# Optimization experiments

Measured on AMD Instinct MI355X. Metric: run time of the kernel, lower is better.

The kernel has to match this reference:

```python
import jax, jax.numpy as jnp
import numpy as np


def setup_inputs() -> dict:
    key = jax.random.key(0)
    ks = jax.random.split(key, 10)
    B, S, I, Hy, H = 16, 4096, 256, 64, 512
    sc = 0.05
    return {
        "x": jax.random.normal(ks[0], (B, S, I), jnp.float32),
        "hidden": jax.random.normal(ks[1], (B, H), jnp.float32),
        "lin0_W": jax.random.normal(ks[2], (Hy, I), jnp.float32) * sc,
        "lin0_b": jax.random.normal(ks[3], (Hy,), jnp.float32) * sc,
        "sig0_W": jax.random.normal(ks[4], (Hy, I), jnp.float32) * sc,
        "sig0_b": jax.random.normal(ks[5], (Hy,), jnp.float32) * sc,
        "fch_W": jax.random.normal(ks[6], (H, Hy), jnp.float32) * sc,
        "fch_b": jax.random.normal(ks[7], (H,), jnp.float32) * sc,
        "fc2_W": jax.random.normal(ks[8], (H, I), jnp.float32) * sc,
        "fc2_b": jax.random.normal(ks[9], (H,), jnp.float32) * sc,
    }


def reference(x, hidden, lin0_W, lin0_b, sig0_W, sig0_b, fch_W, fch_b, fc2_W, fc2_b):
    # GLN sub-network (num_layers=1): relu(linear(x) * sigmoid(linear(x)))
    lin = jnp.einsum('bsi,hi->bsh', x, lin0_W) + lin0_b          # [B,S,Hy]
    gate = jax.nn.sigmoid(jnp.einsum('bsi,hi->bsh', x, sig0_W) + sig0_b)
    g = jax.nn.relu(lin * gate)                                   # [B,S,Hy]
    b = jnp.einsum('bsh,dh->bsd', g, fch_W) + fch_b               # [B,S,H]
    # multihead gating
    sig_alphas = jax.nn.sigmoid(jnp.einsum('bsi,di->bsd', x, fc2_W) + fc2_b)
    b = b * sig_alphas

    # sequential recurrence: h_t = relu(b_t + roll(h_{t-1}, 1, -1)); h_{-1} = hidden
    def step(h, b_t):
        h = jax.nn.relu(b_t + jnp.roll(h, 1, axis=-1))
        return h, h

    b_tmajor = jnp.swapaxes(b, 0, 1)  # [S,B,H]
    last, outs = jax.lax.scan(step, hidden, b_tmajor)
    outputs = jnp.swapaxes(outs, 0, 1)  # [B,S,H]
    return outputs, last
```

## Files before the change

### kernel.cpp

```cpp
#include <hip/hip_runtime.h>

typedef __attribute__((ext_vector_type(4))) float  f32x4;
typedef __attribute__((ext_vector_type(4))) short  s16x4;
typedef __attribute__((ext_vector_type(8))) short  s16x8;
typedef __bf16 bf16x8 __attribute__((ext_vector_type(8)));

#define NBATCH 16
#define SEQ    4096
#define KIN    256
#define HY     64
#define HOUT   512
#define NROWS  (NBATCH*SEQ)
#define LC     32
#define NC     (SEQ/LC)

#define GP(x) ((const __attribute__((address_space(1))) void*)(x))
#define LP(x) ((__attribute__((address_space(3))) void*)(x))

static __device__ __forceinline__ short f2bf(float f) {
  unsigned u = __float_as_uint(f);
  u = u + 0x7FFF + ((u >> 16) & 1);
  return (short)(u >> 16);
}
static __device__ __forceinline__ float bf2f(short h) {
  return __uint_as_float(((unsigned)(unsigned short)h) << 16);
}
static __device__ __forceinline__ f32x4 mfma16(bf16x8 a, bf16x8 b, f32x4 c) {
  return __builtin_amdgcn_mfma_f32_16x16x32_bf16(a, b, c, 0, 0, 0);
}
static __device__ __forceinline__ bf16x8 ldfrag(const short* p) {
  return *reinterpret_cast<const bf16x8*>(p);
}
static __device__ __forceinline__ float fsigmoid(float z) {
  return 1.f / (1.f + __expf(-z));
}

__global__ void prep_w(const float* __restrict__ lin0W, const float* __restrict__ sig0W,
                       const float* __restrict__ fchW,  const float* __restrict__ fc2W,
                       short* __restrict__ W1h, short* __restrict__ W2h,
                       short* __restrict__ Fh,  short* __restrict__ F2h) {
  int i = blockIdx.x * 256 + threadIdx.x;
  if (i < 16384) {
    W1h[i] = f2bf(lin0W[i]);
    W2h[i] = f2bf(sig0W[i]);
  } else if (i < 16384 + 32768) {
    Fh[i - 16384] = f2bf(fchW[i - 16384]);
  } else if (i < 16384 + 32768 + 131072) {
    F2h[i - 49152] = f2bf(fc2W[i - 49152]);
  }
}

__global__ __launch_bounds__(256) void gx(
    const float* __restrict__ x,
    const short* __restrict__ W1h, const short* __restrict__ W2h,
    const float* __restrict__ lin0b, const float* __restrict__ sig0b,
    short* __restrict__ Gh, short* __restrict__ xh) {
  __shared__ __align__(16) short smem[64 * 256 + 64 * 64];
  short* Ah = smem;
  short* gL = smem + 64 * 256;
  int tid = threadIdx.x;
  int row0 = blockIdx.x * 64;
  #pragma unroll
  for (int i = 0; i < 8; ++i) {
    int slot = i * 256 + tid;
    int r = slot >> 5, k8 = slot & 31;
    const float* xp = x + (size_t)(row0 + r) * KIN + k8 * 8;
    f32x4 v0 = *reinterpret_cast<const f32x4*>(xp);
    f32x4 v1 = *reinterpret_cast<const f32x4*>(xp + 4);
    s16x8 hh;
    #pragma unroll
    for (int j = 0; j < 4; ++j) { hh[j] = f2bf(v0[j]); hh[4 + j] = f2bf(v1[j]); }
    *reinterpret_cast<s16x8*>(&Ah[(r * 256 + k8 * 8) ^ ((r & 7) << 3)]) = hh;
    *reinterpret_cast<s16x8*>(xh + (size_t)(row0 + r) * KIN + k8 * 8) = hh;
  }
  __syncthreads();
  int w = tid >> 6, l = tid & 63, lr = l & 15, lg = l >> 4;
  {
    int c = w * 16 + lr;
    f32x4 a1[4], a2[4];
    #pragma unroll
    for (int rt = 0; rt < 4; ++rt) { a1[rt] = (f32x4)0.f; a2[rt] = (f32x4)0.f; }
    #pragma unroll
    for (int ks = 0; ks < 8; ++ks) {
      int kk = ks * 32 + lg * 8;
      bf16x8 b1 = ldfrag(W1h + c * 256 + kk);
      bf16x8 b2 = ldfrag(W2h + c * 256 + kk);
      #pragma unroll
      for (int rt = 0; rt < 4; ++rt) {
        int r = rt * 16 + lr;
        bf16x8 a = ldfrag(&Ah[(r * 256 + kk) ^ ((r & 7) << 3)]);
        a1[rt] = mfma16(b1, a, a1[rt]);
        a2[rt] = mfma16(b2, a, a2[rt]);
      }
    }
    f32x4 blv = *reinterpret_cast<const f32x4*>(lin0b + w * 16 + lg * 4);
    f32x4 bsv = *reinterpret_cast<const f32x4*>(sig0b + w * 16 + lg * 4);
    #pragma unroll
    for (int rt = 0; rt < 4; ++rt) {
      int xrl = rt * 16 + lr;
      s16x4 gg;
      #pragma unroll
      for (int j = 0; j < 4; ++j) {
        float g = (a1[rt][j] + blv[j]) * fsigmoid(a2[rt][j] + bsv[j]);
        gg[j] = f2bf(g > 0.f ? g : 0.f);
      }
      *reinterpret_cast<s16x4*>(&gL[(xrl * 64 + w * 16 + lg * 4) ^ ((xrl & 7) << 3)]) = gg;
    }
  }
  __syncthreads();
  #pragma unroll
  for (int i = 0; i < 2; ++i) {
    int slot = i * 256 + tid;
    int row = slot >> 3, c8 = slot & 7;
    s16x8 v = *reinterpret_cast<const s16x8*>(&gL[(row * 64 + c8 * 8) ^ ((row & 7) << 3)]);
    *reinterpret_cast<s16x8*>(Gh + (size_t)(row0 + row) * HY + c8 * 8) = v;
  }
}

__global__ __launch_bounds__(512, 4) void bg(
    const short* __restrict__ xh, const short* __restrict__ Gh,
    const short* __restrict__ F2h, const short* __restrict__ Fh,
    const float* __restrict__ fchb, const float* __restrict__ fc2b,
    short* __restrict__ Bb) {
  __shared__ __align__(16) short smem[2][16384];
  short* bT = &smem[0][0];
  int tid = threadIdx.x;
  int w = tid >> 6, l = tid & 63;
  int lr = l & 15, lg = l >> 4;
  int r0 = (w >> 1) * 32;
  int c0 = (w & 1) * 64;
  int bid = blockIdx.x;
  int xcd = bid & 7, idx = bid >> 3;
  int colTile = xcd >> 1;
  int rowTile = ((xcd & 1) << 8) + idx;
  int row0 = rowTile * 128;
  int col0 = colTile * 128;

  auto stage = [&](int t, int b) {
    short* As = &smem[b][0];
    short* Bs = &smem[b][8192];
    #pragma unroll
    for (int j = 0; j < 2; ++j) {
      int blk = w * 2 + j;
      int flat = blk * 64 + l;
      int row = flat >> 3, sp = flat & 7;
      int seg = sp ^ (row & 7);
      const short* asrc = (t < 4) ? xh + (size_t)(row0 + row) * KIN + t * 64 + seg * 8
                                  : Gh + (size_t)(row0 + row) * HY + seg * 8;
      const short* bsrc = (t < 4) ? F2h + (size_t)(col0 + row) * KIN + t * 64 + seg * 8
                                  : Fh + (size_t)(col0 + row) * HY + seg * 8;
      __builtin_amdgcn_global_load_lds(GP(asrc), LP(&As[blk * 512]), 16, 0, 0);
      __builtin_amdgcn_global_load_lds(GP(bsrc), LP(&Bs[blk * 512]), 16, 0, 0);
    }
  };
  auto compute = [&](int b, f32x4 (&acc)[2][4]) {
    short* As = &smem[b][0];
    short* Bs = &smem[b][8192];
    #pragma unroll
    for (int ksl = 0; ksl < 2; ++ksl) {
      bf16x8 Af[2], Bf[4];
      #pragma unroll
      for (int i = 0; i < 2; ++i) {
        int row = r0 + i * 16 + lr;
        Af[i] = ldfrag(&As[row * 64 + ((ksl * 32 + lg * 8) ^ ((row & 7) << 3))]);
      }
      #pragma unroll
      for (int i = 0; i < 4; ++i) {
        int col = c0 + i * 16 + lr;
        Bf[i] = ldfrag(&Bs[col * 64 + ((ksl * 32 + lg * 8) ^ ((col & 7) << 3))]);
      }
      #pragma unroll
      for (int rt = 0; rt < 2; ++rt)
        #pragma unroll
        for (int ct = 0; ct < 4; ++ct)
          acc[rt][ct] = mfma16(Af[rt], Bf[ct], acc[rt][ct]);
    }
  };

  f32x4 acc2[2][4], accF[2][4];
  #pragma unroll
  for (int rt = 0; rt < 2; ++rt)
    #pragma unroll
    for (int ct = 0; ct < 4; ++ct) { acc2[rt][ct] = (f32x4)0.f; accF[rt][ct] = (f32x4)0.f; }

  stage(0, 0);
  __syncthreads();
  #pragma unroll
  for (int t = 0; t < 5; ++t) {
    if (t < 4) stage(t + 1, (t + 1) & 1);
    if (t < 4) compute(t & 1, acc2);
    else       compute(t & 1, accF);
    __syncthreads();
  }

  #pragma unroll
  for (int ct = 0; ct < 4; ++ct) {
    int lc = c0 + ct * 16 + lr;
    int col = col0 + lc;
    float bc = fchb[col], b2c = fc2b[col];
    #pragma unroll
    for (int rt = 0; rt < 2; ++rt) {
      int tl0 = r0 + rt * 16 + lg * 4;
      #pragma unroll
      for (int j = 0; j < 4; ++j) {
        int tl = tl0 + j;
        float alpha = fsigmoid(acc2[rt][ct][j] + b2c);
        bT[(tl * 128 + lc) ^ ((tl & 7) << 3)] = f2bf((accF[rt][ct][j] + bc) * alpha);
      }
    }
  }
  __syncthreads();
  #pragma unroll
  for (int i = 0; i < 4; ++i) {
    int slot = i * 512 + tid;
    int row = slot >> 4, c8 = slot & 15;
    s16x8 vv = *reinterpret_cast<const s16x8*>(&bT[(row * 128 + c8 * 8) ^ ((row & 7) << 3)]);
    *reinterpret_cast<s16x8*>(Bb + (size_t)(row0 + row) * HOUT + col0 + c8 * 8) = vv;
  }
}

__global__ __launch_bounds__(64) void scan_passA(const short* __restrict__ Bb,
                                                 float* __restrict__ Cc, float* __restrict__ Sc) {
  int bc = blockIdx.x;
  int l = threadIdx.x;
  int row0 = bc * LC;
  const short* bp = Bb + (size_t)row0 * HOUT + l * 8;
  s16x8 v0 = *reinterpret_cast<const s16x8*>(bp);
  float C[8], S[8];
  #pragma unroll
  for (int i = 0; i < 8; ++i) { S[i] = bf2f(v0[i]); C[i] = 0.f; }
  s16x8 vc = *reinterpret_cast<const s16x8*>(bp + (size_t)HOUT);
  for (int t = 1; t < LC; ++t) {
    s16x8 vn;
    if (t + 1 < LC) vn = *reinterpret_cast<const s16x8*>(bp + (size_t)(t + 1) * HOUT);
    float bb[8];
    #pragma unroll
    for (int i = 0; i < 8; ++i) bb[i] = bf2f(vc[i]);
    float pC = __shfl(C[7], (l + 63) & 63);
    float pS = __shfl(S[7], (l + 63) & 63);
    #pragma unroll
    for (int i = 7; i >= 1; --i) { C[i] = fmaxf(0.f, bb[i] + C[i - 1]); S[i] = bb[i] + S[i - 1]; }
    C[0] = fmaxf(0.f, bb[0] + pC);
    S[0] = bb[0] + pS;
    vc = vn;
  }
  float* cp = Cc + (size_t)bc * HOUT + l * 8;
  float* sp = Sc + (size_t)bc * HOUT + l * 8;
  #pragma unroll
  for (int i = 0; i < 8; ++i) { cp[i] = C[i]; sp[i] = S[i]; }
}

__global__ __launch_bounds__(64) void scan_combine(const float* __restrict__ hidden,
                                                   const float* __restrict__ Cc, const float* __restrict__ Sc,
                                                   float* __restrict__ hIn, float* __restrict__ lastOut) {
  int batch = blockIdx.x;
  int l = threadIdx.x;
  float h[8];
  const float* hp = hidden + batch * HOUT + l * 8;
  #pragma unroll
  for (int i = 0; i < 8; ++i) h[i] = hp[i];
  size_t base0 = ((size_t)batch * NC) * HOUT + l * 8;
  f32x4 pc0[4], pc1[4], ps0[4], ps1[4];
  #pragma unroll
  for (int s = 0; s < 4; ++s) {
    size_t b = base0 + (size_t)s * HOUT;
    pc0[s] = *reinterpret_cast<const f32x4*>(Cc + b);
    pc1[s] = *reinterpret_cast<const f32x4*>(Cc + b + 4);
    ps0[s] = *reinterpret_cast<const f32x4*>(Sc + b);
    ps1[s] = *reinterpret_cast<const f32x4*>(Sc + b + 4);
  }
  for (int cg = 0; cg < NC; cg += 4) {
    #pragma unroll
    for (int s = 0; s < 4; ++s) {
      int c = cg + s;
      size_t base = base0 + (size_t)c * HOUT;
      f32x4 h0, h1;
      #pragma unroll
      for (int i = 0; i < 4; ++i) { h0[i] = h[i]; h1[i] = h[4 + i]; }
      *reinterpret_cast<f32x4*>(hIn + base) = h0;
      *reinterpret_cast<f32x4*>(hIn + base + 4) = h1;
      float hs[8];
      #pragma unroll
      for (int i = 0; i < 8; ++i) hs[i] = __shfl(h[i], (l + 60) & 63);
      #pragma unroll
      for (int i = 0; i < 4; ++i) {
        h[i]     = fmaxf(pc0[s][i], ps0[s][i] + hs[i]);
        h[4 + i] = fmaxf(pc1[s][i], ps1[s][i] + hs[4 + i]);
      }
      if (c + 4 < NC) {
        size_t nb = base + (size_t)4 * HOUT;
        pc0[s] = *reinterpret_cast<const f32x4*>(Cc + nb);
        pc1[s] = *reinterpret_cast<const f32x4*>(Cc + nb + 4);
        ps0[s] = *reinterpret_cast<const f32x4*>(Sc + nb);
        ps1[s] = *reinterpret_cast<const f32x4*>(Sc + nb + 4);
      }
    }
  }
  float* lp = lastOut + batch * HOUT + l * 8;
  #pragma unroll
  for (int i = 0; i < 8; ++i) lp[i] = h[i];
}

__global__ __launch_bounds__(64) void scan_passB(const short* __restrict__ bws,
                                                 const float* __restrict__ hIn,
                                                 float* __restrict__ hout) {
  int bc = blockIdx.x;
  int l = threadIdx.x;
  int row0 = bc * LC;
  const float* hp = hIn + (size_t)bc * HOUT + l * 8;
  float h[8];
  #pragma unroll
  for (int i = 0; i < 8; ++i) h[i] = hp[i];
  s16x8 vc = *reinterpret_cast<const s16x8*>(bws + (size_t)row0 * HOUT + l * 8);
  for (int t = 0; t < LC; ++t) {
    s16x8 vn;
    if (t + 1 < LC)
      vn = *reinterpret_cast<const s16x8*>(bws + (size_t)(row0 + t + 1) * HOUT + l * 8);
    float bb[8];
    #pragma unroll
    for (int i = 0; i < 8; ++i) bb[i] = bf2f(vc[i]);
    float ph = __shfl(h[7], (l + 63) & 63);
    #pragma unroll
    for (int i = 7; i >= 1; --i) h[i] = fmaxf(0.f, bb[i] + h[i - 1]);
    h[0] = fmaxf(0.f, bb[0] + ph);
    f32x4 o0, o1;
    #pragma unroll
    for (int i = 0; i < 4; ++i) { o0[i] = h[i]; o1[i] = h[4 + i]; }
    float* bt = hout + (size_t)(row0 + t) * HOUT + l * 8;
    *reinterpret_cast<f32x4*>(bt) = o0;
    *reinterpret_cast<f32x4*>(bt + 4) = o1;
    vc = vn;
  }
}

extern "C" void kernel_launch(void* const* d_in, const int* in_sizes, int n_in,
                              void* d_out, int out_size, void* d_ws, size_t ws_size,
                              hipStream_t stream) {
  (void)in_sizes; (void)n_in; (void)out_size; (void)ws_size;
  const float* x      = (const float*)d_in[0];
  const float* hidden = (const float*)d_in[1];
  const float* lin0W  = (const float*)d_in[2];
  const float* lin0b  = (const float*)d_in[3];
  const float* sig0W  = (const float*)d_in[4];
  const float* sig0b  = (const float*)d_in[5];
  const float* fchW   = (const float*)d_in[6];
  const float* fchb   = (const float*)d_in[7];
  const float* fc2W   = (const float*)d_in[8];
  const float* fc2b   = (const float*)d_in[9];
  float* outO  = (float*)d_out;
  float* lastO = outO + (size_t)NROWS * HOUT;

  char* wsb = (char*)d_ws;
  size_t off = 0;
  auto alloc = [&](size_t bytes) { char* p = wsb + off; off += (bytes + 255) & ~(size_t)255; return p; };
  float* Cc  = (float*)alloc((size_t)NBATCH * NC * HOUT * 4);
  float* Sc  = (float*)alloc((size_t)NBATCH * NC * HOUT * 4);
  float* hIn = (float*)alloc((size_t)NBATCH * NC * HOUT * 4);
  short* W1h = (short*)alloc(HY * KIN * 2);
  short* W2h = (short*)alloc(HY * KIN * 2);
  short* Fh  = (short*)alloc(HOUT * HY * 2);
  short* F2h = (short*)alloc(HOUT * KIN * 2);
  short* Gh  = (short*)alloc((size_t)NROWS * HY * 2);
  short* xh  = (short*)alloc((size_t)NROWS * KIN * 2);
  short* Bb  = (short*)alloc((size_t)NROWS * HOUT * 2);

  prep_w<<<704, 256, 0, stream>>>(lin0W, sig0W, fchW, fc2W, W1h, W2h, Fh, F2h);
  gx<<<NROWS / 64, 256, 0, stream>>>(x, W1h, W2h, lin0b, sig0b, Gh, xh);
  bg<<<2048, 512, 0, stream>>>(xh, Gh, F2h, Fh, fchb, fc2b, Bb);
  scan_passA<<<NBATCH * NC, 64, 0, stream>>>(Bb, Cc, Sc);
  scan_combine<<<NBATCH, 64, 0, stream>>>(hidden, Cc, Sc, hIn, lastO);
  scan_passB<<<NBATCH * NC, 64, 0, stream>>>(Bb, hIn, outO);
}
```

Before: 168.8 us.

## Fuse scan chunk pass and combine via last-block atomic counter; trim bg loop

Merges the per-chunk scan pass and the per-batch combine kernel into one launch: each chunk block writes its partial carry and sum, then bumps a per-batch atomic counter, and the last block to arrive for a batch runs the sequential combine. This removes one kernel launch and the gap between the two dependent kernels, and lets the combine for one batch start while other batches are still in the chunk pass. The counters are reset inside the weight-prep kernel and the pattern relies on thread fences for visibility. The bg kernel also peels its final compute step out of the pipelined loop, dropping one barrier, and moves the epilogue staging buffer to the other shared buffer to avoid a read-write hazard.

```diff
diff --git a/kernel.cpp b/kernel.cpp
--- a/kernel.cpp
+++ b/kernel.cpp
@@ -38,8 +38,10 @@
 __global__ void prep_w(const float* __restrict__ lin0W, const float* __restrict__ sig0W,
                        const float* __restrict__ fchW,  const float* __restrict__ fc2W,
                        short* __restrict__ W1h, short* __restrict__ W2h,
-                       short* __restrict__ Fh,  short* __restrict__ F2h) {
+                       short* __restrict__ Fh,  short* __restrict__ F2h,
+                       int* __restrict__ cnt) {
   int i = blockIdx.x * 256 + threadIdx.x;
+  if (blockIdx.x == 0 && threadIdx.x < NBATCH) cnt[threadIdx.x] = 0;
   if (i < 16384) {
     W1h[i] = f2bf(lin0W[i]);
     W2h[i] = f2bf(sig0W[i]);
@@ -123,7 +125,7 @@
     const float* __restrict__ fchb, const float* __restrict__ fc2b,
     short* __restrict__ Bb) {
   __shared__ __align__(16) short smem[2][16384];
-  short* bT = &smem[0][0];
+  short* bT = &smem[1][0];
   int tid = threadIdx.x;
   int w = tid >> 6, l = tid & 63;
   int lr = l & 15, lg = l >> 4;
@@ -186,12 +188,12 @@
   stage(0, 0);
   __syncthreads();
   #pragma unroll
-  for (int t = 0; t < 5; ++t) {
-    if (t < 4) stage(t + 1, (t + 1) & 1);
-    if (t < 4) compute(t & 1, acc2);
-    else       compute(t & 1, accF);
+  for (int t = 0; t < 4; ++t) {
+    stage(t + 1, (t + 1) & 1);
+    compute(t & 1, acc2);
     __syncthreads();
   }
+  compute(0, accF);
 
   #pragma unroll
   for (int ct = 0; ct < 4; ++ct) {
@@ -219,42 +221,46 @@
   }
 }
 
-__global__ __launch_bounds__(64) void scan_passA(const short* __restrict__ Bb,
-                                                 float* __restrict__ Cc, float* __restrict__ Sc) {
+__global__ __launch_bounds__(64) void scanAC(
+    const short* __restrict__ Bb, float* __restrict__ Cc, float* __restrict__ Sc,
+    const float* __restrict__ hidden, float* __restrict__ hIn, float* __restrict__ lastOut,
+    int* __restrict__ cnt) {
   int bc = blockIdx.x;
   int l = threadIdx.x;
   int row0 = bc * LC;
-  const short* bp = Bb + (size_t)row0 * HOUT + l * 8;
-  s16x8 v0 = *reinterpret_cast<const s16x8*>(bp);
-  float C[8], S[8];
-  #pragma unroll
-  for (int i = 0; i < 8; ++i) { S[i] = bf2f(v0[i]); C[i] = 0.f; }
-  s16x8 vc = *reinterpret_cast<const s16x8*>(bp + (size_t)HOUT);
-  for (int t = 1; t < LC; ++t) {
-    s16x8 vn;
-    if (t + 1 < LC) vn = *reinterpret_cast<const s16x8*>(bp + (size_t)(t + 1) * HOUT);
-    float bb[8];
-    #pragma unroll
-    for (int i = 0; i < 8; ++i) bb[i] = bf2f(vc[i]);
-    float pC = __shfl(C[7], (l + 63) & 63);
-    float pS = __shfl(S[7], (l + 63) & 63);
-    #pragma unroll
-    for (int i = 7; i >= 1; --i) { C[i] = fmaxf(0.f, bb[i] + C[i - 1]); S[i] = bb[i] + S[i - 1]; }
-    C[0] = fmaxf(0.f, bb[0] + pC);
-    S[0] = bb[0] + pS;
-    vc = vn;
-  }
-  float* cp = Cc + (size_t)bc * HOUT + l * 8;
-  float* sp = Sc + (size_t)bc * HOUT + l * 8;
-  #pragma unroll
-  for (int i = 0; i < 8; ++i) { cp[i] = C[i]; sp[i] = S[i]; }
-}
-
-__global__ __launch_bounds__(64) void scan_combine(const float* __restrict__ hidden,
-                                                   const float* __restrict__ Cc, const float* __restrict__ Sc,
-                                                   float* __restrict__ hIn, float* __restrict__ lastOut) {
-  int batch = blockIdx.x;
-  int l = threadIdx.x;
+  {
+    const short* bp = Bb + (size_t)row0 * HOUT + l * 8;
+    s16x8 v0 = *reinterpret_cast<const s16x8*>(bp);
+    float C[8], S[8];
+    #pragma unroll
+    for (int i = 0; i < 8; ++i) { S[i] = bf2f(v0[i]); C[i] = 0.f; }
+    s16x8 vc = *reinterpret_cast<const s16x8*>(bp + (size_t)HOUT);
+    for (int t = 1; t < LC; ++t) {
+      s16x8 vn;
+      if (t + 1 < LC) vn = *reinterpret_cast<const s16x8*>(bp + (size_t)(t + 1) * HOUT);
+      float bb[8];
+      #pragma unroll
+      for (int i = 0; i < 8; ++i) bb[i] = bf2f(vc[i]);
+      float pC = __shfl(C[7], (l + 63) & 63);
+      float pS = __shfl(S[7], (l + 63) & 63);
+      #pragma unroll
+      for (int i = 7; i >= 1; --i) { C[i] = fmaxf(0.f, bb[i] + C[i - 1]); S[i] = bb[i] + S[i - 1]; }
+      C[0] = fmaxf(0.f, bb[0] + pC);
+      S[0] = bb[0] + pS;
+      vc = vn;
+    }
+    float* cp = Cc + (size_t)bc * HOUT + l * 8;
+    float* sp = Sc + (size_t)bc * HOUT + l * 8;
+    #pragma unroll
+    for (int i = 0; i < 8; ++i) { cp[i] = C[i]; sp[i] = S[i]; }
+  }
+  __threadfence();
+  int batch = bc >> 7;
+  int old = 0;
+  if (l == 0) old = atomicAdd(&cnt[batch], 1);
+  old = __shfl(old, 0);
+  if (old != NC - 1) return;
+  __threadfence();
   float h[8];
   const float* hp = hidden + batch * HOUT + l * 8;
   #pragma unroll
@@ -363,11 +369,11 @@
   short* Gh  = (short*)alloc((size_t)NROWS * HY * 2);
   short* xh  = (short*)alloc((size_t)NROWS * KIN * 2);
   short* Bb  = (short*)alloc((size_t)NROWS * HOUT * 2);
-
-  prep_w<<<704, 256, 0, stream>>>(lin0W, sig0W, fchW, fc2W, W1h, W2h, Fh, F2h);
+  int*   cnt = (int*)alloc(NBATCH * sizeof(int));
+
+  prep_w<<<704, 256, 0, stream>>>(lin0W, sig0W, fchW, fc2W, W1h, W2h, Fh, F2h, cnt);
   gx<<<NROWS / 64, 256, 0, stream>>>(x, W1h, W2h, lin0b, sig0b, Gh, xh);
   bg<<<2048, 512, 0, stream>>>(xh, Gh, F2h, Fh, fchb, fc2b, Bb);
-  scan_passA<<<NBATCH * NC, 64, 0, stream>>>(Bb, Cc, Sc);
-  scan_combine<<<NBATCH, 64, 0, stream>>>(hidden, Cc, Sc, hIn, lastO);
+  scanAC<<<NBATCH * NC, 64, 0, stream>>>(Bb, Cc, Sc, hidden, hIn, lastO, cnt);
   scan_passB<<<NBATCH * NC, 64, 0, stream>>>(Bb, hIn, outO);
 }
```

Result: slower. 248.3 us (+47.1%).
